# Kernel optimization log

Measured on AMD Instinct MI355X. Metric: run time of the kernel, lower is better.

The kernel has to match this reference:

```python
import jax, jax.numpy as jnp
import numpy as np

DIM = 512
NUM_STEPS = 1000
MIN_OMEGA = 0.1
MAX_OMEGA = 10.1
DT = 0.001
INPUT_SCALER = 5.0
BETA1 = 1.0


def setup_inputs() -> dict:
    key = jax.random.key(0)
    k1, k2, k3 = jax.random.split(key, 3)
    B, T, D = 32, NUM_STEPS, DIM
    X_r = jax.random.normal(k1, (B, T, D), dtype=jnp.float32)
    X_i = jax.random.normal(k2, (B, T, D), dtype=jnp.float32)
    # layer parameter: omega_init ~ U(-1, 1), shape (1, dim)
    omegas = jax.random.uniform(k3, (1, D), minval=-1.0, maxval=1.0, dtype=jnp.float32)
    return {"X_r": X_r, "X_i": X_i, "omegas": omegas}


def _hopf(X_r, X_i, omegas):
    # omega mapping: scale to [min, max] Hz then to rad/s
    omega = (omegas * (MAX_OMEGA - MIN_OMEGA) + MIN_OMEGA) * (2.0 * np.pi)  # [1, D]
    B, T, D = X_r.shape
    r0 = jnp.ones((B, D), dtype=X_r.dtype)
    phi0 = jnp.zeros((B, D), dtype=X_r.dtype)

    def step(carry, xs):
        r_t, phis = carry
        xr, xi = xs  # each [B, D]
        input_r = INPUT_SCALER * xr * jnp.cos(phis)
        input_phi = INPUT_SCALER * xi * jnp.sin(phis)
        r_t = r_t + ((1.0 - BETA1 * jnp.square(r_t)) * r_t + input_r) * DT
        phis = phis + (omega - input_phi) * DT
        return (r_t, phis), (r_t, phis)

    xs = (jnp.swapaxes(X_r, 0, 1), jnp.swapaxes(X_i, 0, 1))  # [T, B, D]
    _, (r_seq, phi_seq) = jax.lax.scan(step, (r0, phi0), xs)
    r = jnp.swapaxes(r_seq, 0, 1)    # [B, T, D]
    phi = jnp.swapaxes(phi_seq, 0, 1)
    z_real = r * jnp.cos(phi)
    z_imag = r * jnp.sin(phi)
    return z_real, z_imag


def reference(X_r, X_i, omegas):
    return _hopf(X_r, X_i, omegas)
```

## Files before the change

kernel.cpp:

```cpp
#include <hip/hip_runtime.h>
#include <hip/hip_bf16.h>


#define B 32
#define T 1000
#define D 512
#define DTc 0.001f
#define K_IN 0.005f
#define KREV 7.95774715e-4f
#define U 20
#define NB (T / U)
#define NOPS (U / 4)

typedef float v4f __attribute__((ext_vector_type(4)));
typedef const __attribute__((address_space(1))) float gfloat;
typedef __attribute__((address_space(3))) float lfloat;

#define SCHEDB() __builtin_amdgcn_sched_barrier(0)
#define BAR()    __builtin_amdgcn_s_barrier()
#define W_LGKM0  0xC07F
#define W_VM20   0x4F74
#define W_VM30   0x4F7E
#define W_VM40   0x8F78

__global__ __launch_bounds__(128, 1) void hopf_scan(
    const float* __restrict__ Xr, const float* __restrict__ Xi,
    const float* __restrict__ om,
    float* __restrict__ zr, float* __restrict__ zi) {
    const int tid = threadIdx.x;
    const int bb = blockIdx.x;
    const int b = bb >> 3;
    const int dblk = (bb & 7) << 6;
    const size_t blkoff = (size_t)b * (T * D) + dblk;

    __shared__ __align__(16) float INr[4][U][64];
    __shared__ __align__(16) float INi[4][U][64];
    __shared__ __align__(16) float OUTr[2][U][64];
    __shared__ __align__(16) float OUTi[2][U][64];

    if (tid < 64) {
        const int i = tid;
        const float od = __builtin_fmaf(om[dblk + i], 10.0f, 0.1f) * DTc;
        float r = 1.0f, phi = 0.0f, c = 1.0f, s = 0.0f;

        BAR();
        for (int n = 0; n < NB; ++n) {
            const int ib = n & 3, ob = n & 1;

            float xr[U], xi[U];
#pragma unroll
            for (int t = 0; t < U; ++t) {
                xr[t] = INr[ib][t][i];
                xi[t] = INi[ib][t][i];
            }
            SCHEDB();

            float our[U], oui[U];
#pragma unroll
            for (int t = 0; t < U; ++t) {
                const float omr2 = __builtin_fmaf(-r, r, 1.0f);
                r = __builtin_fmaf(omr2 * r, DTc, r);
                r = __builtin_fmaf(K_IN * xr[t], c, r);
                phi = __builtin_fmaf(-(KREV * xi[t]), s, phi + od);
                s = __builtin_amdgcn_sinf(phi);
                c = __builtin_amdgcn_cosf(phi);
                our[t] = r * c;
                oui[t] = r * s;
            }
            SCHEDB();
#pragma unroll
            for (int t = 0; t < U; ++t) {
                OUTr[ob][t][i] = our[t];
                OUTi[ob][t][i] = oui[t];
            }
            __builtin_amdgcn_s_waitcnt(W_LGKM0);
            SCHEDB();
            BAR();
        }
    } else {
        const int i = tid - 64;
        const int ts = i >> 4;
        const int dq = (i & 15) << 2;
        const float* __restrict__ xr_blk = Xr + blkoff;
        const float* __restrict__ xi_blk = Xi + blkoff;
        float* __restrict__ zr_blk = zr + blkoff;
        float* __restrict__ zi_blk = zi + blkoff;

        auto issueglds = [&](int body) {
            const int buf = body & 3;
#pragma unroll
            for (int k = 0; k < NOPS; ++k) {
                const size_t off = (size_t)(body * U + 4 * k + ts) * D + dq;
                __builtin_amdgcn_global_load_lds((gfloat*)(xr_blk + off),
                                                 (lfloat*)&INr[buf][4 * k][0], 16, 0, 0);
                __builtin_amdgcn_global_load_lds((gfloat*)(xi_blk + off),
                                                 (lfloat*)&INi[buf][4 * k][0], 16, 0, 0);
            }
        };
        auto drainbody = [&](int body) {
            const int ob = body & 1;
#pragma unroll
            for (int k = 0; k < NOPS; ++k) {
                const size_t off = (size_t)(body * U + 4 * k + ts) * D + dq;
                const v4f vr = *reinterpret_cast<const v4f*>(&OUTr[ob][4 * k + ts][dq]);
                const v4f vi = *reinterpret_cast<const v4f*>(&OUTi[ob][4 * k + ts][dq]);
                __builtin_nontemporal_store(vr, reinterpret_cast<v4f*>(zr_blk + off));
                __builtin_nontemporal_store(vi, reinterpret_cast<v4f*>(zi_blk + off));
            }
        };

        issueglds(0);
        issueglds(1);
        issueglds(2);
        __builtin_amdgcn_s_waitcnt(W_VM20);
        SCHEDB();
        BAR();

        for (int n = 0; n < NB; ++n) {
            if (n + 3 < NB) issueglds(n + 3);
            SCHEDB();
            if (n + 1 < NB) {
                const int after = 10 * ((n >= 3) + (n >= 2) +
                                        (n + 2 < NB) + (n + 3 < NB));
                if (after == 40)      __builtin_amdgcn_s_waitcnt(W_VM40);
                else if (after == 30) __builtin_amdgcn_s_waitcnt(W_VM30);
                else                  __builtin_amdgcn_s_waitcnt(W_VM20);
            }
            SCHEDB();
            if (n >= 1) drainbody(n - 1);
            SCHEDB();
            BAR();
        }
        drainbody(NB - 1);
    }
}

extern "C" void kernel_launch(void* const* d_in, const int* in_sizes, int n_in,
                              void* d_out, int out_size, void* d_ws, size_t ws_size,
                              hipStream_t stream) {
    const float* Xr = (const float*)d_in[0];
    const float* Xi = (const float*)d_in[1];
    const float* om = (const float*)d_in[2];
    float* zr = (float*)d_out;
    float* zi = zr + (size_t)B * T * D;

    hopf_scan<<<dim3(B * D / 64), dim3(128), 0, stream>>>(Xr, Xi, om, zr, zi);
}
```

Before: 44.44 us.

## Replace per-step sin/cos with incremental rotation and reorder store drain before wait

The serial recurrence no longer calls hardware sin/cos on the accumulated phase. It advances (cos, sin) by rotating with a small-angle Taylor polynomial of the per-step phase increment, and renormalizes once per block of U steps. This shortens the serial dependency chain by removing transcendental ops. The producer warp now drains outputs before waiting on loads, and its vmcnt thresholds are adjusted to include the stores. Accuracy now relies on the small increment and periodic renormalization, so rounding error builds up over the 1000-step scan.

```diff
diff --git a/kernel.cpp b/kernel.cpp
--- a/kernel.cpp
+++ b/kernel.cpp
@@ -7,10 +7,11 @@
 #define D 512
 #define DTc 0.001f
 #define K_IN 0.005f
-#define KREV 7.95774715e-4f
+#define TWO_PI 6.283185307179586f
 #define U 20
 #define NB (T / U)
 #define NOPS (U / 4)
+#define RING 4
 
 typedef float v4f __attribute__((ext_vector_type(4)));
 typedef const __attribute__((address_space(1))) float gfloat;
@@ -22,6 +23,7 @@
 #define W_VM20   0x4F74
 #define W_VM30   0x4F7E
 #define W_VM40   0x8F78
+#define W_VM50   0xCF72
 
 __global__ __launch_bounds__(128, 1) void hopf_scan(
     const float* __restrict__ Xr, const float* __restrict__ Xi,
@@ -33,15 +35,15 @@
     const int dblk = (bb & 7) << 6;
     const size_t blkoff = (size_t)b * (T * D) + dblk;
 
-    __shared__ __align__(16) float INr[4][U][64];
-    __shared__ __align__(16) float INi[4][U][64];
+    __shared__ __align__(16) float INr[RING][U][64];
+    __shared__ __align__(16) float INi[RING][U][64];
     __shared__ __align__(16) float OUTr[2][U][64];
     __shared__ __align__(16) float OUTi[2][U][64];
 
     if (tid < 64) {
         const int i = tid;
-        const float od = __builtin_fmaf(om[dblk + i], 10.0f, 0.1f) * DTc;
-        float r = 1.0f, phi = 0.0f, c = 1.0f, s = 0.0f;
+        const float od = __builtin_fmaf(om[dblk + i], 10.0f, 0.1f) * (TWO_PI * DTc);
+        float r = 1.0f, c = 1.0f, s = 0.0f;
 
         BAR();
         for (int n = 0; n < NB; ++n) {
@@ -55,23 +57,26 @@
             }
             SCHEDB();
 
-            float our[U], oui[U];
 #pragma unroll
             for (int t = 0; t < U; ++t) {
+                const float m   = K_IN * xi[t];
+                const float dlt = __builtin_fmaf(-m, s, od);
+                const float q   = dlt * dlt;
+                const float pc  = __builtin_fmaf(q, __builtin_fmaf(q, 4.16666667e-2f, -0.5f), 1.0f);
+                const float ps  = dlt * __builtin_fmaf(q, -1.66666667e-1f, 1.0f);
                 const float omr2 = __builtin_fmaf(-r, r, 1.0f);
                 r = __builtin_fmaf(omr2 * r, DTc, r);
                 r = __builtin_fmaf(K_IN * xr[t], c, r);
-                phi = __builtin_fmaf(-(KREV * xi[t]), s, phi + od);
-                s = __builtin_amdgcn_sinf(phi);
-                c = __builtin_amdgcn_cosf(phi);
-                our[t] = r * c;
-                oui[t] = r * s;
+                const float cn = __builtin_fmaf(-s, ps, c * pc);
+                const float sn = __builtin_fmaf(c, ps, s * pc);
+                c = cn; s = sn;
+                OUTr[ob][t][i] = r * c;
+                OUTi[ob][t][i] = r * s;
             }
-            SCHEDB();
-#pragma unroll
-            for (int t = 0; t < U; ++t) {
-                OUTr[ob][t][i] = our[t];
-                OUTi[ob][t][i] = oui[t];
+            {
+                const float n2 = __builtin_fmaf(c, c, s * s);
+                const float h = __builtin_fmaf(-0.5f, n2, 1.5f);
+                c *= h; s *= h;
             }
             __builtin_amdgcn_s_waitcnt(W_LGKM0);
             SCHEDB();
@@ -119,15 +124,16 @@
         for (int n = 0; n < NB; ++n) {
             if (n + 3 < NB) issueglds(n + 3);
             SCHEDB();
+            if (n >= 1) drainbody(n - 1);
+            SCHEDB();
             if (n + 1 < NB) {
-                const int after = 10 * ((n >= 3) + (n >= 2) +
+                const int after = 10 * ((n >= 1) + (n >= 2) + (n >= 3) +
                                         (n + 2 < NB) + (n + 3 < NB));
-                if (after == 40)      __builtin_amdgcn_s_waitcnt(W_VM40);
+                if (after >= 50)      __builtin_amdgcn_s_waitcnt(W_VM50);
+                else if (after == 40) __builtin_amdgcn_s_waitcnt(W_VM40);
                 else if (after == 30) __builtin_amdgcn_s_waitcnt(W_VM30);
                 else                  __builtin_amdgcn_s_waitcnt(W_VM20);
             }
-            SCHEDB();
-            if (n >= 1) drainbody(n - 1);
             SCHEDB();
             BAR();
         }
```

Result: slower. 54.26 us (+22.1%).
